# Kernel tuning notes

Measured on AMD Instinct MI355X. Metric: run time of the kernel, lower is better.

The kernel has to match this reference:

```python
import jax, jax.numpy as jnp
import numpy as np

D = 1024      # d_model
H = 16        # nhead
DH = D // H   # d_head = 64
DC = D // 4   # d_compress = 256
HID = 2048    # dim_feedforward (SwiGLU hidden)
G = 2         # num_groups
EPG = 4       # experts_per_gp
E = G * EPG   # num_experts = 8
TOPK = 2
EPS = 1e-6
B, T = 2, 2048


def _rope_sincos(t, dh):
    inv_freq = 1.0 / (10000.0 ** (jnp.arange(0, dh, 2, dtype=jnp.float32) / dh))
    ang = jnp.arange(t, dtype=jnp.float32)[:, None] * inv_freq[None, :]  # [T, dh/2]
    return jnp.sin(ang), jnp.cos(ang)


def _apply_rope(x, sin, cos):
    # x: [B, H, T, DH]; sin/cos: [T, DH/2] broadcast over B,H
    x1 = x[..., ::2]
    x2 = x[..., 1::2]
    r = jnp.stack([x1 * cos - x2 * sin, x1 * sin + x2 * cos], axis=-1)
    return r.reshape(x.shape)


def _swiglu(x):
    a, b = jnp.split(x, 2, axis=-1)
    return jax.nn.silu(a) * b


def _rmsnorm(x, w):
    return x * jax.lax.rsqrt(jnp.mean(x * x, axis=-1, keepdims=True) + EPS) * w


def reference(src, Wq, Wk_c, Wv_c, Wk, Wv, Wo,
              W_shared_in, W_shared_out, W1_shared, W2_experts,
              Wg_gate, We_gate, group_bias, expert_bias, norm1_w, norm2_w):
    Bb, Tt, C = src.shape
    # ---- Latent attention (K/V compressed to d_c then re-expanded) ----
    q = (src @ Wq).reshape(Bb, Tt, H, DH).transpose(0, 2, 1, 3)
    k = ((src @ Wk_c) @ Wk).reshape(Bb, Tt, H, DH).transpose(0, 2, 1, 3)
    v = ((src @ Wv_c) @ Wv).reshape(Bb, Tt, H, DH).transpose(0, 2, 1, 3)
    sin, cos = _rope_sincos(Tt, DH)
    q = _apply_rope(q, sin, cos)
    k = _apply_rope(k, sin, cos)
    attn = jnp.einsum('bhqd,bhkd->bhqk', q, k) / np.sqrt(DH).astype(np.float32)
    attn = jax.nn.softmax(attn, axis=-1)
    sa = jnp.einsum('bhqk,bhkd->bhqd', attn, v)
    sa = sa.transpose(0, 2, 1, 3).reshape(Bb, Tt, C) @ Wo
    x = _rmsnorm(src + sa, norm1_w)

    # ---- Hierarchical MoE FFN ----
    S = Bb * Tt
    flat = x.reshape(S, C)
    shared = _swiglu(flat @ W_shared_in) @ W_shared_out          # [S, C]
    g_probs = jax.nn.softmax(flat @ Wg_gate + group_bias, -1)    # [S, G]
    g_idx = jnp.argmax(g_probs, axis=-1)                          # [S]
    e_logits = flat @ We_gate + expert_bias                       # [S, E]
    e_group = jnp.arange(E) // EPG
    in_group = e_group[None, :] == g_idx[:, None]                 # [S, E]
    e_probs = jax.nn.softmax(jnp.where(in_group, e_logits, -jnp.inf), -1)
    g_prob = jnp.take_along_axis(g_probs, g_idx[:, None], axis=1)  # [S, 1]
    p_expert = e_probs * g_prob
    topv, topi = jax.lax.top_k(p_expert, TOPK)                    # [S, K]
    # dense combine weights: zero for non-selected experts (same math as dispatch loop)
    w = jnp.zeros((S, E), flat.dtype).at[jnp.arange(S)[:, None], topi].set(topv)
    h = _swiglu(flat @ W1_shared)                                 # [S, HID] (w1 shared by all experts)
    routed = jnp.zeros_like(shared)
    for e in range(E):  # fixed small expert count
        routed = routed + (h @ W2_experts[e]) * w[:, e:e + 1]
    out = x + (shared + routed).reshape(Bb, Tt, C)
    return _rmsnorm(out, norm2_w)


def setup_inputs() -> dict:
    key = jax.random.key(0)
    ks = jax.random.split(key, 14)
    s = 0.02
    return {
        'src': jax.random.normal(ks[0], (B, T, D), jnp.float32),
        'Wq': jax.random.normal(ks[1], (D, D), jnp.float32) * s,
        'Wk_c': jax.random.normal(ks[2], (D, DC), jnp.float32) * s,
        'Wv_c': jax.random.normal(ks[3], (D, DC), jnp.float32) * s,
        'Wk': jax.random.normal(ks[4], (DC, D), jnp.float32) * s,
        'Wv': jax.random.normal(ks[5], (DC, D), jnp.float32) * s,
        'Wo': jax.random.normal(ks[6], (D, D), jnp.float32) * s,
        'W_shared_in': jax.random.normal(ks[7], (D, 2 * HID), jnp.float32) * s,
        'W_shared_out': jax.random.normal(ks[8], (HID, D), jnp.float32) * s,
        'W1_shared': jax.random.normal(ks[9], (D, 2 * HID), jnp.float32) * s,
        'W2_experts': jax.random.normal(ks[10], (E, HID, D), jnp.float32) * s,
        'Wg_gate': jax.random.normal(ks[11], (D, G), jnp.float32) * s,
        'We_gate': jax.random.normal(ks[12], (D, E), jnp.float32) * s,
        'group_bias': jnp.zeros((G,), jnp.float32),
        'expert_bias': jnp.zeros((E,), jnp.float32),
        'norm1_w': jnp.ones((D,), jnp.float32),
        'norm2_w': jnp.ones((D,), jnp.float32),
    }
```

## Files before the change

kernel.cpp:

```cpp
#include <hip/hip_runtime.h>
#include <math.h>

#define D_    1024
#define H_    16
#define DH_   64
#define DC_   256
#define HID_  2048
#define E_    8
#define B_    2
#define T_    2048
#define S_    4096
#define EPS_  1e-6f
#define QKVW_ 3072

typedef unsigned short u16;
typedef short bf16x8 __attribute__((ext_vector_type(8)));
typedef float f32x4 __attribute__((ext_vector_type(4)));

__device__ __forceinline__ float b2f(u16 u) {
    return __uint_as_float(((unsigned int)u) << 16);
}
__device__ __forceinline__ u16 f2b(float f) {
    unsigned int u = __float_as_uint(f);
    u += 0x7FFF + ((u >> 16) & 1);
    return (u16)(u >> 16);
}
__device__ __forceinline__ void g2l16(const u16* g, u16* l) {
    __builtin_amdgcn_global_load_lds(
        (const __attribute__((address_space(1))) void*)g,
        (__attribute__((address_space(3))) void*)l, 16, 0, 0);
}

__global__ __launch_bounds__(256) void conv_t(const float* __restrict__ in,
                                              u16* __restrict__ out,
                                              int K, int N,
                                              long inZ, long outZ, int perm) {
    in  += (long)blockIdx.z * inZ;
    out += (long)blockIdx.z * outZ;
    __shared__ float t[32][33];
    const int n0 = blockIdx.x * 32, k0 = blockIdx.y * 32;
    int src_n0 = n0;
    if (perm) {
        int t64 = n0 >> 6;
        src_n0 = ((n0 & 63) == 0) ? t64 * 32 : (N / 2 + t64 * 32);
    }
    const int tx = threadIdx.x & 31, ty = threadIdx.x >> 5;
#pragma unroll
    for (int i = 0; i < 4; i++)
        t[ty + 8 * i][tx] = in[(long)(k0 + ty + 8 * i) * N + src_n0 + tx];
    __syncthreads();
#pragma unroll
    for (int i = 0; i < 4; i++)
        out[(long)(n0 + ty + 8 * i) * K + k0 + tx] = f2b(t[tx][ty + 8 * i]);
}

__global__ __launch_bounds__(256) void vt_conv(const u16* __restrict__ qkv,
                                               u16* __restrict__ vt) {
    __shared__ u16 t[32][34];
    const int bh = blockIdx.z;
    const int b = bh >> 4, h = bh & 15;
    const int t0 = blockIdx.x * 32, d0 = blockIdx.y * 32;
    const int tx = threadIdx.x & 31, ty = threadIdx.x >> 5;
#pragma unroll
    for (int i = 0; i < 4; i++)
        t[ty + 8 * i][tx] =
            qkv[((long)b * T_ + t0 + ty + 8 * i) * QKVW_ + 2048 + h * 64 + d0 + tx];
    __syncthreads();
#pragma unroll
    for (int i = 0; i < 4; i++)
        vt[((long)bh * 64 + d0 + ty + 8 * i) * T_ + t0 + tx] = t[tx][ty + 8 * i];
}

__global__ __launch_bounds__(256) void convert_bf16(const float* __restrict__ in,
                                                    u16* __restrict__ out, int n4) {
    int i = blockIdx.x * 256 + threadIdx.x;
    if (i >= n4) return;
    float4 f = ((const float4*)in)[i];
    ushort4 o;
    o.x = f2b(f.x); o.y = f2b(f.y); o.z = f2b(f.z); o.w = f2b(f.w);
    ((ushort4*)out)[i] = o;
}

template<int OUTMODE>
__global__ __launch_bounds__(256) void gemm_bf16(const u16* __restrict__ A,
                                                 const u16* __restrict__ Bt,
                                                 void* __restrict__ Cp,
                                                 int N, int K, int ldo,
                                                 void* __restrict__ Cp2) {
    __shared__ u16 As[128 * 32];
    __shared__ u16 Bs[128 * 32];
    const int tid  = threadIdx.x;
    const int lane = tid & 63;
    const int wv   = tid >> 6;
    const int wm   = wv >> 1, wn = wv & 1;
    const long row0 = (long)blockIdx.y * 128;
    const long col0 = (long)blockIdx.x * 128;
    const int Klocal = K / gridDim.z;
    const long koff  = (long)blockIdx.z * Klocal;

    f32x4 acc[4][4];
#pragma unroll
    for (int i = 0; i < 4; i++)
#pragma unroll
        for (int j = 0; j < 4; j++) acc[i][j] = (f32x4){0.f, 0.f, 0.f, 0.f};

    const int sr = tid >> 2;
    const int sc = (tid & 3) << 3;
    const u16* Ag  = A  + (row0 + sr) * (long)K + koff + sc;
    const u16* Ag2 = Ag + 64 * (long)K;
    const u16* Bg  = Bt + (col0 + sr) * (long)K + koff + sc;
    const u16* Bg2 = Bg + 64 * (long)K;
    u16* lA  = As + tid * 8;
    u16* lA2 = As + 2048 + tid * 8;
    u16* lB  = Bs + tid * 8;
    u16* lB2 = Bs + 2048 + tid * 8;

    const int fl = lane & 15;
    const int fk = (lane >> 4) << 3;
    const u16* ArA = As + (wm * 64 + fl) * 32 + fk;
    const u16* BrB = Bs + (wn * 64 + fl) * 32 + fk;

    for (int k0 = 0; k0 < Klocal; k0 += 32) {
        __syncthreads();
        g2l16(Ag + k0, lA);
        g2l16(Ag2 + k0, lA2);
        g2l16(Bg + k0, lB);
        g2l16(Bg2 + k0, lB2);
        __syncthreads();
        bf16x8 af[4], bfr[4];
#pragma unroll
        for (int mi = 0; mi < 4; mi++) af[mi]  = *(const bf16x8*)(ArA + mi * 512);
#pragma unroll
        for (int ni = 0; ni < 4; ni++) bfr[ni] = *(const bf16x8*)(BrB + ni * 512);
#pragma unroll
        for (int mi = 0; mi < 4; mi++)
#pragma unroll
            for (int ni = 0; ni < 4; ni++)
                acc[mi][ni] = __builtin_amdgcn_mfma_f32_16x16x32_bf16(
                    af[mi], bfr[ni], acc[mi][ni], 0, 0, 0);
    }

    const int cr = (lane >> 4) << 2;
    const int cc = lane & 15;
#pragma unroll
    for (int mi = 0; mi < 4; mi++) {
#pragma unroll
        for (int r = 0; r < 4; r++) {
            long grow = row0 + wm * 64 + mi * 16 + cr + r;
            if (OUTMODE == 3) {
                u16* outb = (u16*)Cp + (long)(blockIdx.x >> 5) * S_ * HID_;
                u16* hrow = outb + grow * ldo + (blockIdx.x & 31) * 64 + wn * 32;
#pragma unroll
                for (int ni = 0; ni < 2; ni++) {
                    float a = acc[mi][ni][r], b = acc[mi][ni + 2][r];
                    float sig = 1.f / (1.f + __expf(-a));
                    hrow[ni * 16 + cc] = f2b(a * sig * b);
                }
            } else {
#pragma unroll
                for (int ni = 0; ni < 4; ni++) {
                    long gcol = col0 + wn * 64 + ni * 16 + cc;
                    float v = acc[mi][ni][r];
                    if (OUTMODE == 1)      ((u16*)Cp)[grow * ldo + gcol] = f2b(v);
                    else if (OUTMODE == 2) ((u16*)Cp)[gcol * ldo + grow] = f2b(v);
                    else {
                        float* basep = (float*)(blockIdx.z ? Cp2 : Cp);
                        basep[grow * ldo + gcol] = v;
                    }
                }
            }
        }
    }
}

__global__ __launch_bounds__(256) void routed_gemm(const u16* __restrict__ Hh,
                                                   const u16* __restrict__ W2T,
                                                   const int* __restrict__ list,
                                                   const float* __restrict__ wlist,
                                                   const int* __restrict__ bases,
                                                   const int* __restrict__ counts,
                                                   float* __restrict__ Cout) {
    const int e    = blockIdx.y >> 5;
    const int tile = blockIdx.y & 31;
    const int cnt  = counts[e];
    if (tile * 128 >= cnt) return;
    const int base = bases[e];

    __shared__ u16 As[128 * 32];
    __shared__ u16 Bs[128 * 32];
    __shared__ int   toks[128];
    __shared__ float wrow[128];

    const int tid = threadIdx.x;
    if (tid < 128) {
        int ridx = tile * 128 + tid;
        if (ridx < cnt) { toks[tid] = list[base + ridx]; wrow[tid] = wlist[base + ridx]; }
        else            { toks[tid] = -1;                wrow[tid] = 0.f; }
    }
    __syncthreads();

    const int lane = tid & 63;
    const int wv   = tid >> 6;
    const int wm   = wv >> 1, wn = wv & 1;
    const long col0 = (long)blockIdx.x * 128;

    f32x4 acc[4][4];
#pragma unroll
    for (int i = 0; i < 4; i++)
#pragma unroll
        for (int j = 0; j < 4; j++) acc[i][j] = (f32x4){0.f, 0.f, 0.f, 0.f};

    const int sr = tid >> 2;
    const int sc = (tid & 3) << 3;
    const int t1 = toks[sr], t2 = toks[sr + 64];
    const u16* Ag  = Hh + (long)(t1 < 0 ? 0 : t1) * HID_ + sc;
    const u16* Ag2 = Hh + (long)(t2 < 0 ? 0 : t2) * HID_ + sc;
    const u16* Bg  = W2T + (long)e * D_ * HID_ + (col0 + sr) * (long)HID_ + sc;
    const u16* Bg2 = Bg + 64 * (long)HID_;
    u16* lA  = As + tid * 8;
    u16* lA2 = As + 2048 + tid * 8;
    u16* lB  = Bs + tid * 8;
    u16* lB2 = Bs + 2048 + tid * 8;

    const int fl = lane & 15;
    const int fk = (lane >> 4) << 3;
    const u16* ArA = As + (wm * 64 + fl) * 32 + fk;
    const u16* BrB = Bs + (wn * 64 + fl) * 32 + fk;

    for (int k0 = 0; k0 < HID_; k0 += 32) {
        __syncthreads();
        g2l16(Ag + k0, lA);
        g2l16(Ag2 + k0, lA2);
        g2l16(Bg + k0, lB);
        g2l16(Bg2 + k0, lB2);
        __syncthreads();
        bf16x8 af[4], bfr[4];
#pragma unroll
        for (int mi = 0; mi < 4; mi++) af[mi]  = *(const bf16x8*)(ArA + mi * 512);
#pragma unroll
        for (int ni = 0; ni < 4; ni++) bfr[ni] = *(const bf16x8*)(BrB + ni * 512);
#pragma unroll
        for (int mi = 0; mi < 4; mi++)
#pragma unroll
            for (int ni = 0; ni < 4; ni++)
                acc[mi][ni] = __builtin_amdgcn_mfma_f32_16x16x32_bf16(
                    af[mi], bfr[ni], acc[mi][ni], 0, 0, 0);
    }

    const int cr = (lane >> 4) << 2;
    const int cc = lane & 15;
#pragma unroll
    for (int mi = 0; mi < 4; mi++) {
#pragma unroll
        for (int r = 0; r < 4; r++) {
            int rr = wm * 64 + mi * 16 + cr + r;
            int tk = toks[rr];
            if (tk < 0) continue;
            float wvw = wrow[rr];
            float* crow = Cout + (long)tk * D_ + col0 + wn * 64;
#pragma unroll
            for (int ni = 0; ni < 4; ni++)
                atomicAdd(crow + ni * 16 + cc, acc[mi][ni][r] * wvw);
        }
    }
}

__global__ __launch_bounds__(256) void rope_table(float2* __restrict__ tab) {
    int idx = blockIdx.x * 256 + threadIdx.x;
    int t = idx >> 5, i = idx & 31;
    float ang = (float)t * powf(10000.f, -(float)i / 32.f);
    float sn, cs;
    sincosf(ang, &sn, &cs);
    tab[idx] = make_float2(sn, cs);
}

__global__ __launch_bounds__(256) void rope_apply(u16* __restrict__ qkv,
                                                  const float2* __restrict__ tab) {
    long p = (long)blockIdx.x * 256 + threadIdx.x;
    int s  = (int)(p >> 8);
    int c8 = (int)(p & 255) << 3;
    int t  = s & (T_ - 1);
    const float2* tp = tab + t * 32 + ((c8 & 63) >> 1);
    u16* px = qkv + (long)s * QKVW_ + c8;
    bf16x8 v = *(const bf16x8*)px;
    bf16x8 o;
#pragma unroll
    for (int j = 0; j < 4; j++) {
        float x1 = b2f((u16)v[2 * j]), x2 = b2f((u16)v[2 * j + 1]);
        float2 sc = tp[j];
        o[2 * j]     = (short)f2b(x1 * sc.y - x2 * sc.x);
        o[2 * j + 1] = (short)f2b(x1 * sc.x + x2 * sc.y);
    }
    *(bf16x8*)px = o;
}

__global__ __launch_bounds__(512) void attn_kernel(const u16* __restrict__ qkv,
                                                   const u16* __restrict__ vtg,
                                                   u16* __restrict__ sab) {
    __shared__ u16 Ks[128 * 64];
    __shared__ u16 Vs[64 * 128];
    __shared__ u16 Ps[8][16 * 128];
    const int tid  = threadIdx.x;
    const int lane = tid & 63;
    const int w    = tid >> 6;
    const int flat = blockIdx.x + (blockIdx.y << 4);
    const int virt = ((flat & 7) << 6) | (flat >> 3);
    const int qt = virt & 15;
    const int bh = virt >> 4;
    const int b  = bh >> 4, h = bh & 15;
    const long tok0 = (long)b * T_ + qt * 128;
    const int fl = lane & 15;
    const int fq = lane >> 4;

    bf16x8 qf0, qf1;
    {
        const u16* qp = qkv + (tok0 + w * 16 + fl) * QKVW_ + h * 64 + fq * 8;
        qf0 = *(const bf16x8*)qp;
        qf1 = *(const bf16x8*)(qp + 32);
    }

    const u16* kb0 = qkv + ((long)b * T_) * QKVW_ + 1024 + h * 64;
    const u16* vb0 = vtg + ((long)bh * 64) * T_;

    const int kr0 = tid >> 3,         kgg = tid & 7;
    const int kr1 = (tid + 512) >> 3;
    const int vr0 = tid >> 4,         vgg = tid & 15;
    const int vr1 = (tid + 512) >> 4;
    const u16* kp0 = kb0 + (long)kr0 * QKVW_ + ((kgg ^ (kr0 & 7)) << 3);
    const u16* kp1 = kb0 + (long)kr1 * QKVW_ + ((kgg ^ (kr1 & 7)) << 3);
    const u16* vp0 = vb0 + (long)vr0 * T_ + ((vgg ^ (vr0 & 15)) << 3);
    const u16* vp1 = vb0 + (long)vr1 * T_ + ((vgg ^ (vr1 & 15)) << 3);
    u16* kl0 = Ks + tid * 8;
    u16* kl1 = Ks + (tid + 512) * 8;
    u16* vl0 = Vs + tid * 8;
    u16* vl1 = Vs + (tid + 512) * 8;

    bf16x8 kreg0, kreg1, vreg0, vreg1;
    auto stage_load = [&](int kt) {
        const long ko = (long)kt * 128 * QKVW_;
        const int  vo = kt * 128;
        kreg0 = *(const bf16x8*)(kp0 + ko);
        kreg1 = *(const bf16x8*)(kp1 + ko);
        vreg0 = *(const bf16x8*)(vp0 + vo);
        vreg1 = *(const bf16x8*)(vp1 + vo);
    };
    auto stage_write = [&]() {
        *(bf16x8*)kl0 = kreg0;
        *(bf16x8*)kl1 = kreg1;
        *(bf16x8*)vl0 = vreg0;
        *(bf16x8*)vl1 = vreg1;
    };

    float m_[4], l_[4];
    f32x4 oacc[4];
#pragma unroll
    for (int i = 0; i < 4; i++) {
        m_[i] = -1e30f; l_[i] = 0.f;
        oacc[i] = (f32x4){0.f, 0.f, 0.f, 0.f};
    }

    stage_load(0);
    stage_write();
    __syncthreads();

    for (int kt = 0; kt < T_ / 128; kt++) {
        const bool pf = (kt + 1 < T_ / 128);
        if (pf) stage_load(kt + 1);

        f32x4 sacc[8];
#pragma unroll
        for (int ni = 0; ni < 8; ni++) sacc[ni] = (f32x4){0.f, 0.f, 0.f, 0.f};
        __builtin_amdgcn_s_setprio(1);
#pragma unroll
        for (int ks = 0; ks < 2; ks++) {
            bf16x8 qq = ks ? qf1 : qf0;
#pragma unroll
            for (int ni = 0; ni < 8; ni++) {
                bf16x8 kf = *(const bf16x8*)(Ks + (ni * 16 + fl) * 64 +
                                             (((ks * 4 + fq) ^ (fl & 7)) << 3));
                sacc[ni] = __builtin_amdgcn_mfma_f32_16x16x32_bf16(qq, kf, sacc[ni], 0, 0, 0);
            }
        }
        __builtin_amdgcn_s_setprio(0);

        float rmax[4];
#pragma unroll
        for (int r = 0; r < 4; r++) {
            float mm = sacc[0][r];
#pragma unroll
            for (int ni = 1; ni < 8; ni++) mm = fmaxf(mm, sacc[ni][r]);
            rmax[r] = mm * 0.125f;
        }
#pragma unroll
        for (int off = 1; off < 16; off <<= 1)
#pragma unroll
            for (int r = 0; r < 4; r++) rmax[r] = fmaxf(rmax[r], __shfl_xor(rmax[r], off));

        bool grow = false;
        float nm[4];
#pragma unroll
        for (int r = 0; r < 4; r++) {
            nm[r] = fmaxf(m_[r], rmax[r]);
            grow = grow || (rmax[r] > m_[r] + 8.f);
        }
        if (__any(grow)) {
#pragma unroll
            for (int r = 0; r < 4; r++) {
                float a = __expf(m_[r] - nm[r]);
                m_[r] = nm[r];
                l_[r] *= a;
#pragma unroll
                for (int ni = 0; ni < 4; ni++) oacc[ni][r] *= a;
            }
        }

        float psum[4];
#pragma unroll
        for (int r = 0; r < 4; r++) psum[r] = 0.f;
        u16* pst = Ps[w];
#pragma unroll
        for (int ni = 0; ni < 8; ni++) {
            int colg = ni * 2 + (fl >> 3);
            int cl   = fl & 7;
#pragma unroll
            for (int r = 0; r < 4; r++) {
                int row = fq * 4 + r;
                float p = __expf(sacc[ni][r] * 0.125f - m_[r]);
                psum[r] += p;
                pst[row * 128 + ((colg ^ (row & 15)) << 3) + cl] = f2b(p);
            }
        }
#pragma unroll
        for (int off = 1; off < 16; off <<= 1)
#pragma unroll
            for (int r = 0; r < 4; r++) psum[r] += __shfl_xor(psum[r], off);
#pragma unroll
        for (int r = 0; r < 4; r++) l_[r] += psum[r];

        __builtin_amdgcn_s_setprio(1);
#pragma unroll
        for (int ks = 0; ks < 4; ks++) {
            bf16x8 pfr = *(const bf16x8*)(pst + fl * 128 +
                                          (((ks * 4 + fq) ^ fl) << 3));
#pragma unroll
            for (int ni = 0; ni < 4; ni++) {
                bf16x8 vf = *(const bf16x8*)(Vs + (ni * 16 + fl) * 128 +
                                             (((ks * 4 + fq) ^ fl) << 3));
                oacc[ni] = __builtin_amdgcn_mfma_f32_16x16x32_bf16(pfr, vf, oacc[ni], 0, 0, 0);
            }
        }
        __builtin_amdgcn_s_setprio(0);

        __syncthreads();
        if (pf) {
            stage_write();
            __syncthreads();
        }
    }

#pragma unroll
    for (int r = 0; r < 4; r++) {
        float inv = 1.f / l_[r];
        u16* op = sab + (tok0 + w * 16 + fq * 4 + r) * D_ + h * 64 + fl;
#pragma unroll
        for (int ni = 0; ni < 4; ni++) op[ni * 16] = f2b(oacc[ni][r] * inv);
    }
}

template<int BF>
__global__ __launch_bounds__(256) void rmsnorm_res(const float* __restrict__ a,
                                                   const float* __restrict__ b,
                                                   const float* __restrict__ b2,
                                                   const float* __restrict__ w,
                                                   float* __restrict__ outf,
                                                   u16* __restrict__ outb) {
    const int s = blockIdx.x;
    const float* ar = a + (long)s * D_;
    const float* br = b + (long)s * D_;
    const float* cr2 = b2 + (long)s * D_;
    float y[4];
    float ss = 0.f;
#pragma unroll
    for (int kx = 0; kx < 4; kx++) {
        int j = threadIdx.x + kx * 256;
        y[kx] = ar[j] + br[j] + cr2[j];
        ss += y[kx] * y[kx];
    }
    __shared__ float red[4];
#pragma unroll
    for (int off = 32; off > 0; off >>= 1) ss += __shfl_down(ss, off);
    int lane = threadIdx.x & 63, wv = threadIdx.x >> 6;
    if (lane == 0) red[wv] = ss;
    __syncthreads();
    float tot = red[0] + red[1] + red[2] + red[3];
    float scl = rsqrtf(tot / (float)D_ + EPS_);
    float* orow = outf + (long)s * D_;
#pragma unroll
    for (int kx = 0; kx < 4; kx++) {
        int j = threadIdx.x + kx * 256;
        float v = y[kx] * scl * w[j];
        orow[j] = v;
        if (BF) outb[(long)s * D_ + j] = f2b(v);
    }
}

__global__ __launch_bounds__(256) void gate_kernel(const float* __restrict__ x,
                                                   const float* __restrict__ Wg,
                                                   const float* __restrict__ We,
                                                   const float* __restrict__ gb,
                                                   const float* __restrict__ eb,
                                                   int* __restrict__ tok_e,
                                                   float* __restrict__ tok_w) {
    const int wave = threadIdx.x >> 6;
    const int lane = threadIdx.x & 63;
    const int s = blockIdx.x * 4 + wave;
    const float* xr = x + (long)s * D_;
    float g0 = 0.f, g1 = 0.f;
    float ee[8];
#pragma unroll
    for (int e = 0; e < 8; e++) ee[e] = 0.f;
    for (int j = lane; j < D_; j += 64) {
        float xv = xr[j];
        g0 += xv * Wg[j * 2 + 0];
        g1 += xv * Wg[j * 2 + 1];
#pragma unroll
        for (int e = 0; e < 8; e++) ee[e] += xv * We[j * 8 + e];
    }
#pragma unroll
    for (int off = 32; off > 0; off >>= 1) {
        g0 += __shfl_down(g0, off);
        g1 += __shfl_down(g1, off);
#pragma unroll
        for (int e = 0; e < 8; e++) ee[e] += __shfl_down(ee[e], off);
    }
    if (lane == 0) {
        g0 += gb[0];
        g1 += gb[1];
        int gidx = (g1 > g0) ? 1 : 0;
        float gm = fmaxf(g0, g1);
        float p0 = expf(g0 - gm), p1 = expf(g1 - gm);
        float gprob = (gidx ? p1 : p0) / (p0 + p1);
        int base = gidx * 4;
        float pe[4];
        float em = -1e30f;
#pragma unroll
        for (int i = 0; i < 4; i++) {
            pe[i] = ee[base + i] + eb[base + i];
            em = fmaxf(em, pe[i]);
        }
        float sum = 0.f;
#pragma unroll
        for (int i = 0; i < 4; i++) { pe[i] = expf(pe[i] - em); sum += pe[i]; }
        float inv = gprob / sum;
#pragma unroll
        for (int i = 0; i < 4; i++) pe[i] *= inv;
        int i1 = 0;
        for (int i = 1; i < 4; i++) if (pe[i] > pe[i1]) i1 = i;
        int i2 = -1;
        for (int i = 0; i < 4; i++) {
            if (i == i1) continue;
            if (i2 < 0 || pe[i] > pe[i2]) i2 = i;
        }
        tok_e[s * 2 + 0] = base + i1;
        tok_e[s * 2 + 1] = base + i2;
        tok_w[s * 2 + 0] = pe[i1];
        tok_w[s * 2 + 1] = pe[i2];
    }
}

__global__ __launch_bounds__(256) void route_build(const int* __restrict__ tok_e,
                                                   const float* __restrict__ tok_w,
                                                   int* __restrict__ counts_g,
                                                   int* __restrict__ bases_g,
                                                   int* __restrict__ list,
                                                   float* __restrict__ wlist) {
    __shared__ int cnt[E_], bas[E_], cur[E_];
    const int tid = threadIdx.x;
    if (tid < E_) cnt[tid] = 0;
    __syncthreads();
    for (int i = tid; i < 2 * S_; i += 256) atomicAdd(&cnt[tok_e[i]], 1);
    __syncthreads();
    if (tid == 0) {
        int acc = 0;
        for (int e = 0; e < E_; e++) { bas[e] = acc; cur[e] = acc; acc += cnt[e]; }
    }
    __syncthreads();
    if (tid < E_) { counts_g[tid] = cnt[tid]; bases_g[tid] = bas[tid]; }
    for (int i = tid; i < 2 * S_; i += 256) {
        int e = tok_e[i];
        int p = atomicAdd(&cur[e], 1);
        list[p] = i >> 1;
        wlist[p] = tok_w[i];
    }
}

extern "C" void kernel_launch(void* const* d_in, const int* in_sizes, int n_in,
                              void* d_out, int out_size, void* d_ws, size_t ws_size,
                              hipStream_t stream) {
    const float* src  = (const float*)d_in[0];
    const float* Wq   = (const float*)d_in[1];
    const float* Wk_c = (const float*)d_in[2];
    const float* Wv_c = (const float*)d_in[3];
    const float* Wk   = (const float*)d_in[4];
    const float* Wv   = (const float*)d_in[5];
    const float* Wo   = (const float*)d_in[6];
    const float* Wsin = (const float*)d_in[7];
    const float* Wsout= (const float*)d_in[8];
    const float* W1   = (const float*)d_in[9];
    const float* W2   = (const float*)d_in[10];
    const float* Wg   = (const float*)d_in[11];
    const float* We   = (const float*)d_in[12];
    const float* gb   = (const float*)d_in[13];
    const float* eb   = (const float*)d_in[14];
    const float* n1w  = (const float*)d_in[15];
    const float* n2w  = (const float*)d_in[16];
    float* out = (float*)d_out;

    const size_t MB = 1u << 20;
    char* w8 = (char*)d_ws;
    u16*  qkv   = (u16*)(w8);
    u16*  vtg   = (u16*)(w8 + 24 * MB);
    float* oproj0 = (float*)(w8);
    float* oproj1 = (float*)(w8 + 16 * MB);
    u16*  w2t   = (u16*)(w8);
    u16*  WkcB  = (u16*)(w8 + 24 * MB);
    u16*  WvcB  = (u16*)(w8 + 24 * MB + 512 * 1024);
    u16*  WkTs  = (u16*)(w8 + 25 * MB);
    u16*  WvTs  = (u16*)(w8 + 25 * MB + 512 * 1024);
    u16*  sab   = (u16*)(w8 + 32 * MB);
    float* tokw = (float*)(w8 + 32 * MB);
    float* wlist = tokw + 2 * S_;
    int* toke   = (int*)(wlist + 2 * S_);
    int* list   = toke + 2 * S_;
    int* counts = list + 2 * S_;
    int* bases  = counts + E_;
    float* x1   = (float*)(w8 + 40 * MB);
    float* ffn0 = (float*)(w8 + 56 * MB);
    u16*  x1b   = (u16*)(w8 + 72 * MB);
    u16*  hbuf  = (u16*)(w8 + 80 * MB);
    u16*  srcb  = (u16*)(w8 + 96 * MB);
    float2* rtab= (float2*)(w8 + 104 * MB);
    u16*  hbuf2 = (u16*)(w8 + 96 * MB);
    u16*  WqkvT = (u16*)(w8 + 112 * MB);
    u16*  WsoutT= (u16*)(w8 + 112 * MB);
    u16*  WoT   = (u16*)(w8 + 118 * MB);
    u16*  WsinT = (u16*)(w8 + 120 * MB);
    u16*  W1T   = (u16*)(w8 + 128 * MB);
    float* ffn1 = (float*)(w8 + 120 * MB);

    dim3 blk(256);

    conv_t<<<dim3(32, 32), blk, 0, stream>>>(Wq, WqkvT, 1024, 1024, 0, 0, 0);
    convert_bf16<<<dim3(D_ * DC_ / 4 / 256), blk, 0, stream>>>(Wk_c, WkcB, D_ * DC_ / 4);
    convert_bf16<<<dim3(D_ * DC_ / 4 / 256), blk, 0, stream>>>(Wv_c, WvcB, D_ * DC_ / 4);
    conv_t<<<dim3(32, 8), blk, 0, stream>>>(Wk, WkTs, 256, 1024, 0, 0, 0);
    conv_t<<<dim3(32, 8), blk, 0, stream>>>(Wv, WvTs, 256, 1024, 0, 0, 0);
    gemm_bf16<2><<<dim3(8, 8), blk, 0, stream>>>(WkcB, WkTs, WqkvT + 1024 * 1024, 1024, 256, 1024, nullptr);
    gemm_bf16<2><<<dim3(8, 8), blk, 0, stream>>>(WvcB, WvTs, WqkvT + 2048 * 1024, 1024, 256, 1024, nullptr);

    convert_bf16<<<dim3(S_ * D_ / 4 / 256), blk, 0, stream>>>(src, srcb, S_ * D_ / 4);

    gemm_bf16<1><<<dim3(24, 32), blk, 0, stream>>>(srcb, WqkvT, qkv, QKVW_, 1024, QKVW_, nullptr);

    conv_t<<<dim3(32, 32), blk, 0, stream>>>(Wo, WoT, 1024, 1024, 0, 0, 0);
    conv_t<<<dim3(128, 32), blk, 0, stream>>>(Wsin, WsinT, 1024, 4096, 0, 0, 1);
    conv_t<<<dim3(32, 64), blk, 0, stream>>>(Wsout, WsoutT, 2048, 1024, 0, 0, 0);
    conv_t<<<dim3(128, 32), blk, 0, stream>>>(W1, W1T, 1024, 4096, 0, 0, 1);

    rope_table<<<dim3(T_ * 32 / 256), blk, 0, stream>>>(rtab);
    rope_apply<<<dim3(S_ * 2048 / 8 / 256), blk, 0, stream>>>(qkv, rtab);

    vt_conv<<<dim3(T_ / 32, 2, B_ * H_), blk, 0, stream>>>(qkv, vtg);
    attn_kernel<<<dim3(T_ / 128, B_ * H_), dim3(512), 0, stream>>>(qkv, vtg, sab);

    gemm_bf16<5><<<dim3(8, 32, 2), blk, 0, stream>>>(sab, WoT, oproj0, 1024, 1024, 1024, oproj1);
    rmsnorm_res<1><<<dim3(S_), blk, 0, stream>>>(src, oproj0, oproj1, n1w, x1, x1b);

    gemm_bf16<3><<<dim3(64, 32), blk, 0, stream>>>(x1b, WsinT, hbuf, 8192, 1024, 2048, nullptr);

    gemm_bf16<5><<<dim3(8, 32, 2), blk, 0, stream>>>(hbuf, WsoutT, ffn0, 1024, 2048, 1024, ffn1);

    gate_kernel<<<dim3(S_ / 4), blk, 0, stream>>>(x1, Wg, We, gb, eb, toke, tokw);
    route_build<<<dim3(1), blk, 0, stream>>>(toke, tokw, counts, bases, list, wlist);

    conv_t<<<dim3(32, 64, 8), blk, 0, stream>>>(W2, w2t, 2048, 1024,
                                                (long)HID_ * D_, (long)D_ * HID_, 0);
    routed_gemm<<<dim3(8, E_ * 32), blk, 0, stream>>>(hbuf2, w2t, list, wlist,
                                                      bases, counts, ffn0);

    rmsnorm_res<0><<<dim3(S_), blk, 0, stream>>>(x1, ffn0, ffn1, n2w, out, (u16*)nullptr);
}
```

Measured before the change: 671.5 us.

## Add 256x256-tile double-buffered GEMM for QKV and fused SwiGLU input projections

```diff
diff --git a/kernel.cpp b/kernel.cpp
--- a/kernel.cpp
+++ b/kernel.cpp
@@ -147,9 +147,101 @@
 #pragma unroll
         for (int r = 0; r < 4; r++) {
             long grow = row0 + wm * 64 + mi * 16 + cr + r;
+#pragma unroll
+            for (int ni = 0; ni < 4; ni++) {
+                long gcol = col0 + wn * 64 + ni * 16 + cc;
+                float v = acc[mi][ni][r];
+                if (OUTMODE == 1)      ((u16*)Cp)[grow * ldo + gcol] = f2b(v);
+                else if (OUTMODE == 2) ((u16*)Cp)[gcol * ldo + grow] = f2b(v);
+                else {
+                    float* basep = (float*)(blockIdx.z ? Cp2 : Cp);
+                    basep[grow * ldo + gcol] = v;
+                }
+            }
+        }
+    }
+}
+
+template<int OUTMODE>
+__global__ __launch_bounds__(512) void gemm256(const u16* __restrict__ A,
+                                               const u16* __restrict__ Bt,
+                                               void* __restrict__ Cp,
+                                               int K, int ldo) {
+    __shared__ u16 As[2][256 * 64];
+    __shared__ u16 Bs[2][256 * 64];
+    const int tid  = threadIdx.x;
+    const int lane = tid & 63;
+    const int w    = tid >> 6;
+    const int wr   = w >> 2, wc = w & 3;
+    const long row0 = (long)blockIdx.y * 256;
+    const long col0 = (long)blockIdx.x * 256;
+
+    f32x4 acc[8][4];
+#pragma unroll
+    for (int i = 0; i < 8; i++)
+#pragma unroll
+        for (int j = 0; j < 4; j++) acc[i][j] = (f32x4){0.f, 0.f, 0.f, 0.f};
+
+    const int srow = tid >> 3;
+    const int sgS  = ((tid & 7) ^ (srow & 7)) << 3;
+    const u16* Ag = A  + (row0 + srow) * (long)K + sgS;
+    const u16* Bg = Bt + (col0 + srow) * (long)K + sgS;
+
+    const int fl = lane & 15;
+    const int fq = lane >> 4;
+    const int aoff = (wr * 128 + fl) * 64;
+    const int boff = (wc * 64 + fl) * 64;
+
+#define STAGE256(j, buf) do {                                             \
+        const long ko_ = (long)(j) * 64;                                  \
+        u16* la_ = As[buf] + tid * 8;                                     \
+        u16* lb_ = Bs[buf] + tid * 8;                                     \
+        _Pragma("unroll")                                                 \
+        for (int rr_ = 0; rr_ < 4; rr_++)                                 \
+            g2l16(Ag + (long)rr_ * 64 * K + ko_, la_ + rr_ * 4096);       \
+        _Pragma("unroll")                                                 \
+        for (int rr_ = 0; rr_ < 4; rr_++)                                 \
+            g2l16(Bg + (long)rr_ * 64 * K + ko_, lb_ + rr_ * 4096);       \
+    } while (0)
+
+    STAGE256(0, 0);
+    __syncthreads();
+    const int NT = K >> 6;
+    for (int j = 0; j < NT; j++) {
+        const int buf = j & 1;
+        if (j + 1 < NT) STAGE256(j + 1, buf ^ 1);
+        const u16* ab = As[buf];
+        const u16* bb = Bs[buf];
+#pragma unroll
+        for (int ks = 0; ks < 2; ks++) {
+            const int sw = ((ks * 4 + fq) ^ (fl & 7)) << 3;
+            bf16x8 af[8], bfr[4];
+#pragma unroll
+            for (int mi = 0; mi < 8; mi++)
+                af[mi] = *(const bf16x8*)(ab + aoff + mi * 1024 + sw);
+#pragma unroll
+            for (int ni = 0; ni < 4; ni++)
+                bfr[ni] = *(const bf16x8*)(bb + boff + ni * 1024 + sw);
+#pragma unroll
+            for (int mi = 0; mi < 8; mi++)
+#pragma unroll
+                for (int ni = 0; ni < 4; ni++)
+                    acc[mi][ni] = __builtin_amdgcn_mfma_f32_16x16x32_bf16(
+                        af[mi], bfr[ni], acc[mi][ni], 0, 0, 0);
+        }
+        __syncthreads();
+    }
+
+    const int cr = fq << 2;
+    const int cc = fl;
+#pragma unroll
+    for (int mi = 0; mi < 8; mi++) {
+#pragma unroll
+        for (int r = 0; r < 4; r++) {
+            long grow = row0 + wr * 128 + mi * 16 + cr + r;
             if (OUTMODE == 3) {
-                u16* outb = (u16*)Cp + (long)(blockIdx.x >> 5) * S_ * HID_;
-                u16* hrow = outb + grow * ldo + (blockIdx.x & 31) * 64 + wn * 32;
+                u16* outb = (u16*)Cp + (long)(blockIdx.x >> 4) * S_ * HID_;
+                u16* hrow = outb + grow * ldo + (blockIdx.x & 15) * 128 + wc * 32;
 #pragma unroll
                 for (int ni = 0; ni < 2; ni++) {
                     float a = acc[mi][ni][r], b = acc[mi][ni + 2][r];
@@ -159,18 +251,13 @@
             } else {
 #pragma unroll
                 for (int ni = 0; ni < 4; ni++) {
-                    long gcol = col0 + wn * 64 + ni * 16 + cc;
-                    float v = acc[mi][ni][r];
-                    if (OUTMODE == 1)      ((u16*)Cp)[grow * ldo + gcol] = f2b(v);
-                    else if (OUTMODE == 2) ((u16*)Cp)[gcol * ldo + grow] = f2b(v);
-                    else {
-                        float* basep = (float*)(blockIdx.z ? Cp2 : Cp);
-                        basep[grow * ldo + gcol] = v;
-                    }
+                    long gcol = col0 + wc * 64 + ni * 16 + cc;
+                    ((u16*)Cp)[grow * ldo + gcol] = f2b(acc[mi][ni][r]);
                 }
             }
         }
     }
+#undef STAGE256
 }
 
 __global__ __launch_bounds__(256) void routed_gemm(const u16* __restrict__ Hh,
@@ -660,7 +747,7 @@
 
     convert_bf16<<<dim3(S_ * D_ / 4 / 256), blk, 0, stream>>>(src, srcb, S_ * D_ / 4);
 
-    gemm_bf16<1><<<dim3(24, 32), blk, 0, stream>>>(srcb, WqkvT, qkv, QKVW_, 1024, QKVW_, nullptr);
+    gemm256<1><<<dim3(QKVW_ / 256, S_ / 256), dim3(512), 0, stream>>>(srcb, WqkvT, qkv, 1024, QKVW_);
 
     conv_t<<<dim3(32, 32), blk, 0, stream>>>(Wo, WoT, 1024, 1024, 0, 0, 0);
     conv_t<<<dim3(128, 32), blk, 0, stream>>>(Wsin, WsinT, 1024, 4096, 0, 0, 1);
@@ -676,7 +763,7 @@
     gemm_bf16<5><<<dim3(8, 32, 2), blk, 0, stream>>>(sab, WoT, oproj0, 1024, 1024, 1024, oproj1);
     rmsnorm_res<1><<<dim3(S_), blk, 0, stream>>>(src, oproj0, oproj1, n1w, x1, x1b);
 
-    gemm_bf16<3><<<dim3(64, 32), blk, 0, stream>>>(x1b, WsinT, hbuf, 8192, 1024, 2048, nullptr);
+    gemm256<3><<<dim3(8192 / 256, S_ / 256), dim3(512), 0, stream>>>(x1b, WsinT, hbuf, 1024, 2048);
 
     gemm_bf16<5><<<dim3(8, 32, 2), blk, 0, stream>>>(hbuf, WsoutT, ffn0, 1024, 2048, 1024, ffn1);
 
```

Result: faster. 631.7 us (-5.9%).
